# Kernel optimization log

Hardware: AMD Instinct MI355X
Metric: run time of the kernel (lower is better)

Reference implementation:

```python
import jax, jax.numpy as jnp
import numpy as np

B, C, H, W_SP = 4, 64, 64, 64
CI = C // 2  # inter_channels = 32
DEPTH = 64
EPS = 1e-5


def conv2d(x, w, b, pad=0, dil=1):
    out = jax.lax.conv_general_dilated(
        x, w, window_strides=(1, 1),
        padding=[(pad, pad), (pad, pad)],
        rhs_dilation=(dil, dil),
        dimension_numbers=('NCHW', 'OIHW', 'NCHW'))
    return out + b[None, :, None, None]


def setup_inputs() -> dict:
    key = jax.random.key(0)
    ks = iter(jax.random.split(key, 32))
    nrm = lambda shp, s=0.01: jax.random.normal(next(ks), shp, jnp.float32) * s
    inp = {
        'x': jax.random.normal(next(ks), (B, C, H, W_SP), jnp.float32),
        # NonlocalBlock params (init: normal(0, 0.01), bias 0)
        'g_w': nrm((CI, C, 1, 1)), 'g_b': jnp.zeros((CI,), jnp.float32),
        'theta_w': nrm((CI, C, 1, 1)), 'theta_b': jnp.zeros((CI,), jnp.float32),
        'phi_w': nrm((CI, C, 1, 1)), 'phi_b': jnp.zeros((CI,), jnp.float32),
        'Wz_w': nrm((C, CI, 1, 1)), 'Wz_b': jnp.zeros((C,), jnp.float32),
        'bn_g': jax.random.normal(next(ks), (C,), jnp.float32),  # normal_(W[1].weight, 0) -> std 1
        'bn_b': jnp.zeros((C,), jnp.float32),
        # ASPP params (torch default kaiming init approximated by small normals)
        'a_mean_w': nrm((DEPTH, C, 1, 1), 0.05), 'a_mean_b': jnp.zeros((DEPTH,), jnp.float32),
        'a1_w': nrm((DEPTH, C, 1, 1), 0.05), 'a1_b': jnp.zeros((DEPTH,), jnp.float32),
        'a3_w': nrm((DEPTH, C, 3, 3), 0.02), 'a3_b': jnp.zeros((DEPTH,), jnp.float32),
        'a5_w': nrm((DEPTH, C, 3, 3), 0.02), 'a5_b': jnp.zeros((DEPTH,), jnp.float32),
        'a7_w': nrm((DEPTH, C, 3, 3), 0.02), 'a7_b': jnp.zeros((DEPTH,), jnp.float32),
        'out_w': nrm((DEPTH, DEPTH * 5, 1, 1), 0.02), 'out_b': jnp.zeros((DEPTH,), jnp.float32),
    }
    return inp


def _forward(x, g_w, g_b, theta_w, theta_b, phi_w, phi_b, Wz_w, Wz_b, bn_g, bn_b,
             a_mean_w, a_mean_b, a1_w, a1_b, a3_w, a3_b, a5_w, a5_b, a7_w, a7_b,
             out_w, out_b):
    b, c, h, w = x.shape
    n = h * w
    # ---- NonlocalBlock: global self-attention ----
    g_x = conv2d(x, g_w, g_b).reshape(b, CI, n).transpose(0, 2, 1)       # [B,N,Ci]
    theta_x = conv2d(x, theta_w, theta_b).reshape(b, CI, n).transpose(0, 2, 1)  # [B,N,Ci]
    phi_x = conv2d(x, phi_w, phi_b).reshape(b, CI, n)                    # [B,Ci,N]
    f = jnp.einsum('bqc,bck->bqk', theta_x, phi_x)                       # [B,N,N]
    f_div_C = jax.nn.softmax(f, axis=2)
    y = jnp.einsum('bqk,bkc->bqc', f_div_C, g_x)                         # [B,N,Ci]
    y = y.transpose(0, 2, 1).reshape(b, CI, h, w)
    wy = conv2d(y, Wz_w, Wz_b)
    # BatchNorm (eval: running_mean=0, running_var=1)
    wy = wy * (bn_g / jnp.sqrt(1.0 + EPS))[None, :, None, None] + bn_b[None, :, None, None]
    z = wy + x
    # ---- ASPP ----
    img = jnp.mean(z, axis=(2, 3), keepdims=True)                        # [B,C,1,1]
    img = conv2d(img, a_mean_w, a_mean_b)                                # [B,D,1,1]
    img = jnp.broadcast_to(img, (b, DEPTH, h, w))  # bilinear upsample of 1x1 is constant
    b1 = conv2d(z, a1_w, a1_b)
    b3 = conv2d(z, a3_w, a3_b, pad=3, dil=3)
    b5 = conv2d(z, a5_w, a5_b, pad=5, dil=5)
    b7 = conv2d(z, a7_w, a7_b, pad=7, dil=7)
    cat = jnp.concatenate([img, b1, b3, b5, b7], axis=1)                 # [B,5D,H,W]
    return conv2d(cat, out_w, out_b)                                     # [B,D,H,W]


def reference(x, g_w, g_b, theta_w, theta_b, phi_w, phi_b, Wz_w, Wz_b, bn_g, bn_b,
              a_mean_w, a_mean_b, a1_w, a1_b, a3_w, a3_b, a5_w, a5_b, a7_w, a7_b,
              out_w, out_b):
    return _forward(x, g_w, g_b, theta_w, theta_b, phi_w, phi_b, Wz_w, Wz_b, bn_g, bn_b,
                    a_mean_w, a_mean_b, a1_w, a1_b, a3_w, a3_b, a5_w, a5_b, a7_w, a7_b,
                    out_w, out_b)
```

## Files before the change

kernel.cpp:

```cpp
#include <hip/hip_runtime.h>


typedef __attribute__((ext_vector_type(8))) short bf16x8;
typedef __attribute__((ext_vector_type(4))) short s16x4;
typedef __attribute__((ext_vector_type(4))) float f32x4;

#define MFMA(a, b, c) __builtin_amdgcn_mfma_f32_16x16x32_bf16((a), (b), (c), 0, 0, 0)

#if __has_builtin(__builtin_amdgcn_exp2f)
#define EXP2(x) __builtin_amdgcn_exp2f(x)
#else
#define EXP2(x) exp2f(x)
#endif

__device__ static inline short f2bf(float f) {
  union { float f; unsigned u; } v; v.f = f;
  unsigned r = v.u + 0x7fffu + ((v.u >> 16) & 1u);
  return (short)(r >> 16);
}
__device__ static inline float bf2f(unsigned short h) {
  union { unsigned u; float f; } v; v.u = ((unsigned)h) << 16;
  return v.f;
}
__device__ static inline s16x4 pk4(f32x4 v) {
  s16x4 r; r.x = f2bf(v.x); r.y = f2bf(v.y); r.z = f2bf(v.z); r.w = f2bf(v.w);
  return r;
}
__device__ static inline unsigned pk2(float f0, float f1) {
  union { float f; unsigned u; } a, b; a.f = f0; b.f = f1;
  return __builtin_amdgcn_perm(b.u, a.u, 0x07060302u);
}
__device__ static inline f32x4 exp24(f32x4 v) {
  f32x4 r; r.x = EXP2(v.x); r.y = EXP2(v.y); r.z = EXP2(v.z); r.w = EXP2(v.w);
  return r;
}

#define QF_PER_B 131072
#define ZPB      389376
#define LOG2E    1.4426950408889634f

__global__ __launch_bounds__(256) void k_setup(
    const float* __restrict__ x,
    const float* __restrict__ tw, const float* __restrict__ tb,
    const float* __restrict__ pw, const float* __restrict__ pb,
    const float* __restrict__ gw, const float* __restrict__ gb,
    const float* __restrict__ out_w, const float* __restrict__ out_b,
    const float* __restrict__ a1_w, const float* __restrict__ a3_w,
    const float* __restrict__ a5_w, const float* __restrict__ a7_w,
    const float* __restrict__ a1_b, const float* __restrict__ a3_b,
    const float* __restrict__ a5_b, const float* __restrict__ a7_b,
    const float* __restrict__ Wz_w, const float* __restrict__ Wz_b,
    const float* __restrict__ bn_g, const float* __restrict__ bn_b,
    const float* __restrict__ am_w,
    unsigned* __restrict__ zp, float* __restrict__ zmean,
    unsigned short* __restrict__ Wfrag, unsigned short* __restrict__ WzF,
    float* __restrict__ bias2,
    unsigned short* __restrict__ thetaB, unsigned short* __restrict__ phiB,
    unsigned short* __restrict__ gB,
    float* __restrict__ am_wT, float* __restrict__ owT0,
    float* __restrict__ cbias) {
  __shared__ union {
    struct { float wsm[4096]; float osm[64 * 65]; } prep;
    struct { float wl[2048]; float bl[32]; } qkv;
  } sm;
  int blk = blockIdx.x, t = threadIdx.x;
  if (blk < 997) {
    if (blk == 996) { if (t < 256) zmean[t] = 0.f; return; }
    int b = blk / 249, loc = blk - b * 249;
    int i = loc * 256 + t;
    if (i >= 63616) return;
    int px = i >> 5, dw = i & 31;
    int row, col;
    if (px < 1092) {
      int r = px / 78; col = px - r * 78;
      row = (r < 7) ? r : r + 64;
    } else {
      int j = px - 1092;
      int r = j / 14; int c = j - r * 14;
      row = r + 7; col = (c < 7) ? c : c + 57;
    }
    zp[b * (ZPB / 2) + (row * 78 + col) * 32 + dw] = 0u;
  } else if (blk < 1027) {
    int pblk = blk - 997;
    if (pblk < 28) {
      int tap = pblk;
      const float* w; int goff, kyx = 0, ksq = 9;
      if (tap == 0)      { w = a1_w; goff = 64;  ksq = 1; }
      else if (tap < 10) { w = a3_w; goff = 128; kyx = tap - 1; }
      else if (tap < 19) { w = a5_w; goff = 192; kyx = tap - 10; }
      else               { w = a7_w; goff = 256; kyx = tap - 19; }
      for (int i = t; i < 4096; i += 256) {
        sm.prep.wsm[i] = w[i * ksq + kyx];
        int d = i >> 6, m = i & 63;
        sm.prep.osm[d * 65 + m] = out_w[d * 320 + goff + m];
      }
      __syncthreads();
      int dt = t >> 6, lane = t & 63, quad = lane >> 4, l15 = lane & 15;
      int d = dt * 16 + l15;
      float acc[16];
      #pragma unroll
      for (int k = 0; k < 16; ++k) acc[k] = 0.f;
      const float* orow = sm.prep.osm + d * 65;
      int c0 = quad * 8;
      for (int m = 0; m < 64; ++m) {
        float o = orow[m];
        const float* wr = sm.prep.wsm + m * 64 + c0;
        #pragma unroll
        for (int cc = 0; cc < 2; ++cc)
          #pragma unroll
          for (int j = 0; j < 8; ++j)
            acc[cc * 8 + j] += o * wr[cc * 32 + j];
      }
      #pragma unroll
      for (int cc = 0; cc < 2; ++cc) {
        bf16x8 v;
        #pragma unroll
        for (int j = 0; j < 8; ++j) v[j] = f2bf(acc[cc * 8 + j]);
        *(bf16x8*)(Wfrag + (((tap * 4 + dt) * 2 + cc) * 64 + lane) * 8) = v;
      }
    } else if (pblk == 28) {
      int ct = t >> 6, lane = t & 63, quad = lane >> 4, l15 = lane & 15;
      int c = ct * 16 + l15;
      float s = bn_g[c] * rsqrtf(1.f + 1e-5f);
      bf16x8 v;
      #pragma unroll
      for (int j = 0; j < 8; ++j) v[j] = f2bf(s * Wz_w[c * 32 + quad * 8 + j]);
      *(bf16x8*)(WzF + (ct * 64 + lane) * 8) = v;
    } else if (t < 64) {
      float s = bn_g[t] * rsqrtf(1.f + 1e-5f);
      bias2[t] = s * Wz_b[t] + bn_b[t];
    }
  } else if (blk < 1219) {
    int qb = blk - 1027;
    int b = qb & 3, pt = (qb >> 2) & 15, proj = qb >> 6;
    const float* w    = proj == 0 ? tw : (proj == 1 ? pw : gw);
    const float* bias = proj == 0 ? tb : (proj == 1 ? pb : gb);
    for (int i = t; i < 2048; i += 256) sm.qkv.wl[i] = w[i];
    if (t < 32) sm.qkv.bl[t] = bias[t];
    __syncthreads();
    int pix = pt*256 + t;
    const float* xp = x + b*64*4096 + pix;
    float acc[32];
    #pragma unroll
    for (int ci = 0; ci < 32; ++ci) acc[ci] = sm.qkv.bl[ci];
    for (int c = 0; c < 64; ++c) {
      float xv = xp[c*4096];
      #pragma unroll
      for (int ci = 0; ci < 32; ++ci) acc[ci] += sm.qkv.wl[ci*64 + c] * xv;
    }
    if (proj == 0) {
      #pragma unroll
      for (int ci = 0; ci < 32; ++ci) acc[ci] *= LOG2E;
    }
    if (proj < 2) {
      unsigned short* base = (proj == 0 ? thetaB : phiB) + b*QF_PER_B
                             + (pix >> 4)*512 + (pix & 15)*8;
      #pragma unroll
      for (int q = 0; q < 4; ++q) {
        bf16x8 v;
        #pragma unroll
        for (int j = 0; j < 8; ++j) v[j] = f2bf(acc[q*8 + j]);
        *(bf16x8*)(base + q*128) = v;
      }
    } else {
      unsigned short* base = gB + b*QF_PER_B + (pix >> 5)*1024
                             + ((pix & 31) >> 3)*128 + (pix & 7);
      #pragma unroll
      for (int ci = 0; ci < 32; ++ci)
        base[(ci >> 4)*512 + (ci & 15)*8] = (unsigned short)f2bf(acc[ci]);
    }
  } else {
    for (int i = t; i < 4096; i += 256) {
      int d = i >> 6, c = i & 63;
      am_wT[c * 64 + d] = am_w[i];
      owT0[c * 64 + d] = out_w[d * 320 + c];
    }
    if (t < 64) {
      float r = out_b[t];
      const float* ow = out_w + t * 320;
      for (int m = 0; m < 64; ++m)
        r += ow[64 + m] * a1_b[m] + ow[128 + m] * a3_b[m]
           + ow[192 + m] * a5_b[m] + ow[256 + m] * a7_b[m];
      cbias[t] = r;
    }
  }
}

__global__ __launch_bounds__(512) void k_attn(
    const unsigned short* __restrict__ thetaB, const unsigned short* __restrict__ phiB,
    const unsigned short* __restrict__ gB, const unsigned short* __restrict__ WzF,
    const float* __restrict__ bias2, const float* __restrict__ x,
    unsigned short* __restrict__ z_pad, float* __restrict__ zmean) {
  __shared__ float ypart[8][64][20];
  __shared__ __align__(16) unsigned short plds[8][1152];
  __shared__ __align__(16) unsigned short ytr[4][1280];
  int blk = blockIdx.x;
  int b = blk >> 7, qblk = blk & 127;
  int tid = threadIdx.x;
  int kh = tid >> 6, lane = tid & 63, quad = lane >> 4, l15 = lane & 15;
  const bf16x8* thB = (const bf16x8*)(thetaB + b*QF_PER_B);
  const bf16x8* phF = (const bf16x8*)(phiB + b*QF_PER_B);
  const bf16x8* gF  = (const bf16x8*)(gB + b*QF_PER_B);
  bf16x8 th0 = thB[(qblk*2 + 0)*64 + lane];
  bf16x8 th1 = thB[(qblk*2 + 1)*64 + lane];
  bf16x8 ones;
  #pragma unroll
  for (int j = 0; j < 8; ++j) ones[j] = (short)0x3F80;
  const f32x4 z4 = {0.f, 0.f, 0.f, 0.f};
  f32x4 acc00 = z4, acc01 = z4, acc10 = z4, acc11 = z4;
  f32x4 accL0 = z4, accL1 = z4;
  unsigned short* pl = &plds[kh][0];
  unsigned short* r0p = pl + l15*36 + quad*4;
  unsigned short* r1p = pl + 576 + l15*36 + quad*4;
  const unsigned short* q0p = pl + l15*36 + quad*8;
  const unsigned short* q1p = pl + 576 + l15*36 + quad*8;
  int kt0 = kh*16;
  for (int kt = kt0; kt < kt0 + 16; ++kt) {
    int tbase = kt*128 + lane;
    bf16x8 pf0 = phF[tbase];
    bf16x8 pf1 = phF[tbase + 64];
    bf16x8 gf0 = gF[tbase];
    bf16x8 gf1 = gF[tbase + 64];
    f32x4 s00 = MFMA(pf0, th0, z4);
    f32x4 s10 = MFMA(pf1, th0, z4);
    f32x4 s01 = MFMA(pf0, th1, z4);
    f32x4 s11 = MFMA(pf1, th1, z4);
    f32x4 p00 = exp24(s00), p10 = exp24(s10), p01 = exp24(s01), p11 = exp24(s11);
    uint2 w0; w0.x = pk2(p00.x, p00.y); w0.y = pk2(p00.z, p00.w);
    uint2 w1; w1.x = pk2(p10.x, p10.y); w1.y = pk2(p10.z, p10.w);
    uint2 w2; w2.x = pk2(p01.x, p01.y); w2.y = pk2(p01.z, p01.w);
    uint2 w3; w3.x = pk2(p11.x, p11.y); w3.y = pk2(p11.z, p11.w);
    *(uint2*)(r0p)      = w0;
    *(uint2*)(r0p + 16) = w1;
    *(uint2*)(r1p)      = w2;
    *(uint2*)(r1p + 16) = w3;
    uint2 a0 = *(const uint2*)(q0p);
    uint2 a1 = *(const uint2*)(q0p + 4);
    uint2 b0 = *(const uint2*)(q1p);
    uint2 b1 = *(const uint2*)(q1p + 4);
    union { unsigned u[4]; bf16x8 v; } pb0c, pb1c;
    pb0c.u[0] = a0.x; pb0c.u[1] = a0.y; pb0c.u[2] = a1.x; pb0c.u[3] = a1.y;
    pb1c.u[0] = b0.x; pb1c.u[1] = b0.y; pb1c.u[2] = b1.x; pb1c.u[3] = b1.y;
    acc00 = MFMA(gf0, pb0c.v, acc00);
    acc01 = MFMA(gf1, pb0c.v, acc01);
    acc10 = MFMA(gf0, pb1c.v, acc10);
    acc11 = MFMA(gf1, pb1c.v, acc11);
    accL0 = MFMA(ones, pb0c.v, accL0);
    accL1 = MFMA(ones, pb1c.v, accL1);
  }
  float* yp = &ypart[kh][lane][0];
  *(f32x4*)(yp + 0)  = acc00;
  *(f32x4*)(yp + 4)  = acc01;
  *(f32x4*)(yp + 8)  = acc10;
  *(f32x4*)(yp + 12) = acc11;
  yp[16] = accL0.x; yp[17] = accL1.x;
  __syncthreads();
  if (kh >= 4) return;
  int ct = kh;
  f32x4 a00 = z4, a01 = z4, a10 = z4, a11 = z4;
  float l0 = 0.f, l1 = 0.f;
  #pragma unroll
  for (int k = 0; k < 8; ++k) {
    const float* q = &ypart[k][lane][0];
    a00 += *(const f32x4*)(q + 0);
    a01 += *(const f32x4*)(q + 4);
    a10 += *(const f32x4*)(q + 8);
    a11 += *(const f32x4*)(q + 12);
    l0 += q[16]; l1 += q[17];
  }
  float r0 = 1.f / l0, r1 = 1.f / l1;
  a00 *= r0; a01 *= r0; a10 *= r1; a11 *= r1;
  unsigned short* yl = &ytr[ct][0];
  *(s16x4*)(yl + l15*40 + quad*4)             = pk4(a00);
  *(s16x4*)(yl + l15*40 + 16 + quad*4)        = pk4(a01);
  *(s16x4*)(yl + (16 + l15)*40 + quad*4)      = pk4(a10);
  *(s16x4*)(yl + (16 + l15)*40 + 16 + quad*4) = pk4(a11);
  bf16x8 y0 = *(const bf16x8*)(yl + l15*40 + quad*8);
  bf16x8 y1 = *(const bf16x8*)(yl + (16 + l15)*40 + quad*8);
  bf16x8 wf = ((const bf16x8*)WzF)[ct*64 + lane];
  f32x4 zq0 = MFMA(wf, y0, z4);
  f32x4 zq1 = MFMA(wf, y1, z4);
  int c0 = ct*16 + quad*4;
  f32x4 b2 = *(const f32x4*)(bias2 + c0);
  int q0i = qblk * 32;
  const float* xp0 = x + (b*64 + c0)*4096 + q0i + l15;
  f32x4 s0, s1;
  s0.x = zq0.x + b2.x + xp0[0];
  s0.y = zq0.y + b2.y + xp0[4096];
  s0.z = zq0.z + b2.z + xp0[8192];
  s0.w = zq0.w + b2.w + xp0[12288];
  s1.x = zq1.x + b2.x + xp0[16];
  s1.y = zq1.y + b2.y + xp0[4096 + 16];
  s1.z = zq1.z + b2.z + xp0[8192 + 16];
  s1.w = zq1.w + b2.w + xp0[12288 + 16];
  {
    int q = q0i + l15, h = q >> 6, w = q & 63;
    *(s16x4*)(z_pad + b*ZPB + ((h + 7)*78 + (w + 7))*64 + c0) = pk4(s0);
    q = q0i + 16 + l15; h = q >> 6; w = q & 63;
    *(s16x4*)(z_pad + b*ZPB + ((h + 7)*78 + (w + 7))*64 + c0) = pk4(s1);
  }
  f32x4 zs = s0 + s1;
  #pragma unroll
  for (int m = 1; m < 16; m <<= 1) {
    zs.x += __shfl_xor(zs.x, m);
    zs.y += __shfl_xor(zs.y, m);
    zs.z += __shfl_xor(zs.z, m);
    zs.w += __shfl_xor(zs.w, m);
  }
  if (l15 == 0) {
    atomicAdd(zmean + b*64 + c0 + 0, zs.x);
    atomicAdd(zmean + b*64 + c0 + 1, zs.y);
    atomicAdd(zmean + b*64 + c0 + 2, zs.z);
    atomicAdd(zmean + b*64 + c0 + 3, zs.w);
  }
}

__global__ __launch_bounds__(64) void k_conv(
    const unsigned short* __restrict__ z_pad, const unsigned short* __restrict__ Wfrag,
    const float* __restrict__ zmean, const float* __restrict__ am_wT,
    const float* __restrict__ am_b, const float* __restrict__ owT0,
    const float* __restrict__ cbias, float* __restrict__ out) {
  static constexpr int DYt[28] = {0, -3,-3,-3,0,0,0,3,3,3,
                                     -5,-5,-5,0,0,0,5,5,5,
                                     -7,-7,-7,0,0,0,7,7,7};
  static constexpr int DXt[28] = {0, -3,0,3,-3,0,3,-3,0,3,
                                     -5,0,5,-5,0,5,-5,0,5,
                                     -7,0,7,-7,0,7,-7,0,7};
  int blk = blockIdx.x;
  int b = blk >> 8, h = (blk >> 2) & 63, dt2 = (blk >> 1) & 1, wt2 = blk & 1;
  int lane = threadIdx.x, quad = lane >> 4, l15 = lane & 15;
  float zml = zmean[b*64 + lane] * (1.f / 4096.f);
  float img = am_b[lane];
  for (int c = 0; c < 64; ++c) img += am_wT[c*64 + lane] * __shfl(zml, c);
  float cbd = cbias[lane];
  for (int dd = 0; dd < 64; ++dd) cbd += owT0[dd*64 + lane] * __shfl(img, dd);
  const unsigned short* zb = z_pad + b*ZPB + ((h + 7)*78 + 7)*64 + quad*8;
  const bf16x8* wfp = (const bf16x8*)Wfrag + lane;
  int d0 = dt2*2 + 0, d1 = dt2*2 + 1;
  const f32x4 z4 = {0.f, 0.f, 0.f, 0.f};
  f32x4 acc00 = z4, acc01 = z4, acc10 = z4, acc11 = z4;
  int col0 = ((wt2*2 + 0)*16 + l15)*64;
  int col1 = ((wt2*2 + 1)*16 + l15)*64;
  #pragma unroll
  for (int tap = 0; tap < 28; ++tap) {
    int toff = (DYt[tap]*78 + DXt[tap])*64;
    const unsigned short* zrow = zb + toff;
    #pragma unroll
    for (int cc = 0; cc < 2; ++cc) {
      bf16x8 zf0 = *(const bf16x8*)(zrow + col0 + cc*32);
      bf16x8 zf1 = *(const bf16x8*)(zrow + col1 + cc*32);
      bf16x8 wf0 = wfp[((tap*4 + d0)*2 + cc)*64];
      bf16x8 wf1 = wfp[((tap*4 + d1)*2 + cc)*64];
      acc00 = MFMA(wf0, zf0, acc00);
      acc01 = MFMA(wf0, zf1, acc01);
      acc10 = MFMA(wf1, zf0, acc10);
      acc11 = MFMA(wf1, zf1, acc11);
    }
  }
  int dd0 = d0*16 + quad*4, dd1 = d1*16 + quad*4;
  f32x4 cb0v, cb1v;
  cb0v.x = __shfl(cbd, dd0 + 0); cb0v.y = __shfl(cbd, dd0 + 1);
  cb0v.z = __shfl(cbd, dd0 + 2); cb0v.w = __shfl(cbd, dd0 + 3);
  cb1v.x = __shfl(cbd, dd1 + 0); cb1v.y = __shfl(cbd, dd1 + 1);
  cb1v.z = __shfl(cbd, dd1 + 2); cb1v.w = __shfl(cbd, dd1 + 3);
  acc00 += cb0v; acc01 += cb0v; acc10 += cb1v; acc11 += cb1v;
  float* ob = out + b*262144 + h*64;
  int w0 = (wt2*2 + 0)*16 + l15, w1 = (wt2*2 + 1)*16 + l15;
  ob[(dd0 + 0)*4096 + w0] = acc00.x;
  ob[(dd0 + 1)*4096 + w0] = acc00.y;
  ob[(dd0 + 2)*4096 + w0] = acc00.z;
  ob[(dd0 + 3)*4096 + w0] = acc00.w;
  ob[(dd0 + 0)*4096 + w1] = acc01.x;
  ob[(dd0 + 1)*4096 + w1] = acc01.y;
  ob[(dd0 + 2)*4096 + w1] = acc01.z;
  ob[(dd0 + 3)*4096 + w1] = acc01.w;
  ob[(dd1 + 0)*4096 + w0] = acc10.x;
  ob[(dd1 + 1)*4096 + w0] = acc10.y;
  ob[(dd1 + 2)*4096 + w0] = acc10.z;
  ob[(dd1 + 3)*4096 + w0] = acc10.w;
  ob[(dd1 + 0)*4096 + w1] = acc11.x;
  ob[(dd1 + 1)*4096 + w1] = acc11.y;
  ob[(dd1 + 2)*4096 + w1] = acc11.z;
  ob[(dd1 + 3)*4096 + w1] = acc11.w;
}

extern "C" void kernel_launch(void* const* d_in, const int* in_sizes, int n_in,
                              void* d_out, int out_size, void* d_ws, size_t ws_size,
                              hipStream_t stream) {
  const float* x    = (const float*)d_in[0];
  const float* g_w  = (const float*)d_in[1];
  const float* g_b  = (const float*)d_in[2];
  const float* th_w = (const float*)d_in[3];
  const float* th_b = (const float*)d_in[4];
  const float* ph_w = (const float*)d_in[5];
  const float* ph_b = (const float*)d_in[6];
  const float* Wz_w = (const float*)d_in[7];
  const float* Wz_b = (const float*)d_in[8];
  const float* bn_g = (const float*)d_in[9];
  const float* bn_b = (const float*)d_in[10];
  const float* am_w = (const float*)d_in[11];
  const float* am_b = (const float*)d_in[12];
  const float* a1_w = (const float*)d_in[13];
  const float* a1_b = (const float*)d_in[14];
  const float* a3_w = (const float*)d_in[15];
  const float* a3_b = (const float*)d_in[16];
  const float* a5_w = (const float*)d_in[17];
  const float* a5_b = (const float*)d_in[18];
  const float* a7_w = (const float*)d_in[19];
  const float* a7_b = (const float*)d_in[20];
  const float* out_w = (const float*)d_in[21];
  const float* out_b = (const float*)d_in[22];
  float* out = (float*)d_out;
  char* ws = (char*)d_ws;
  unsigned short* thetaB = (unsigned short*)(ws + 0);
  unsigned short* phiB   = (unsigned short*)(ws + 1048576);
  unsigned short* gB     = (unsigned short*)(ws + 2097152);
  unsigned short* z_pad  = (unsigned short*)(ws + 3145728);
  unsigned short* Wfrag  = (unsigned short*)(ws + 6260736);
  unsigned short* WzF    = (unsigned short*)(ws + 6490112);
  float* zmean           = (float*)(ws + 6494208);
  float* bias2           = (float*)(ws + 6495232);
  float* am_wT           = (float*)(ws + 6495488);
  float* owT0            = (float*)(ws + 6511872);
  float* cbias           = (float*)(ws + 6528256);

  k_setup<<<dim3(1220), dim3(256), 0, stream>>>(
      x, th_w, th_b, ph_w, ph_b, g_w, g_b, out_w, out_b,
      a1_w, a3_w, a5_w, a7_w, a1_b, a3_b, a5_b, a7_b,
      Wz_w, Wz_b, bn_g, bn_b, am_w,
      (unsigned*)z_pad, zmean, Wfrag, WzF, bias2,
      thetaB, phiB, gB, am_wT, owT0, cbias);
  k_attn<<<dim3(512), dim3(512), 0, stream>>>(thetaB, phiB, gB, WzF, bias2, x,
                                              z_pad, zmean);
  k_conv<<<dim3(1024), dim3(64), 0, stream>>>(z_pad, Wfrag, zmean, am_wT, am_b,
                                              owT0, cbias, out);
}
```

Measured before the change: 182.2 us.

## Rebalance kernels: fold padding and weight prep into attention, prefetch operands

Replaces the big setup kernel with a small projection kernel. The halo zeroing and ASPP weight folding become extra blocks of the attention kernel, so they run alongside attention work. Adds register double-buffering of phi/g loads in the attention loop and of z_pad loads in the conv loop. The conv kernel is regrouped into 256-thread blocks, one per output row, and the projection kernel batches its x loads. It also fixes the right-halo column index so the zeroing no longer lands on interior columns, which matters now that zeroing runs concurrently with the z writes.

```diff
diff --git a/kernel.cpp b/kernel.cpp
--- a/kernel.cpp
+++ b/kernel.cpp
@@ -18,10 +18,6 @@
   unsigned r = v.u + 0x7fffu + ((v.u >> 16) & 1u);
   return (short)(r >> 16);
 }
-__device__ static inline float bf2f(unsigned short h) {
-  union { unsigned u; float f; } v; v.u = ((unsigned)h) << 16;
-  return v.f;
-}
 __device__ static inline s16x4 pk4(f32x4 v) {
   s16x4 r; r.x = f2bf(v.x); r.y = f2bf(v.y); r.z = f2bf(v.z); r.w = f2bf(v.w);
   return r;
@@ -39,35 +35,226 @@
 #define ZPB      389376
 #define LOG2E    1.4426950408889634f
 
-__global__ __launch_bounds__(256) void k_setup(
+__global__ __launch_bounds__(256) void k_proj(
     const float* __restrict__ x,
     const float* __restrict__ tw, const float* __restrict__ tb,
     const float* __restrict__ pw, const float* __restrict__ pb,
     const float* __restrict__ gw, const float* __restrict__ gb,
+    const float* __restrict__ Wz_w, const float* __restrict__ Wz_b,
+    const float* __restrict__ bn_g, const float* __restrict__ bn_b,
+    unsigned short* __restrict__ thetaB, unsigned short* __restrict__ phiB,
+    unsigned short* __restrict__ gB, unsigned short* __restrict__ WzF,
+    float* __restrict__ bias2, float* __restrict__ zmean) {
+  __shared__ float wl[2048];
+  __shared__ float bl[32];
+  int blk = blockIdx.x, t = threadIdx.x;
+  if (blk < 192) {
+    int b = blk & 3, pt = (blk >> 2) & 15, proj = blk >> 6;
+    const float* w    = proj == 0 ? tw : (proj == 1 ? pw : gw);
+    const float* bias = proj == 0 ? tb : (proj == 1 ? pb : gb);
+    for (int i = t; i < 2048; i += 256) wl[i] = w[i];
+    if (t < 32) bl[t] = bias[t];
+    __syncthreads();
+    int pix = pt*256 + t;
+    const float* xp = x + b*64*4096 + pix;
+    float acc[32];
+    #pragma unroll
+    for (int ci = 0; ci < 32; ++ci) acc[ci] = bl[ci];
+    for (int c0 = 0; c0 < 64; c0 += 16) {
+      float xv[16];
+      #pragma unroll
+      for (int k = 0; k < 16; ++k) xv[k] = xp[(c0 + k)*4096];
+      #pragma unroll
+      for (int k = 0; k < 16; ++k)
+        #pragma unroll
+        for (int ci = 0; ci < 32; ++ci) acc[ci] += wl[ci*64 + c0 + k] * xv[k];
+    }
+    if (proj == 0) {
+      #pragma unroll
+      for (int ci = 0; ci < 32; ++ci) acc[ci] *= LOG2E;
+    }
+    if (proj < 2) {
+      unsigned short* base = (proj == 0 ? thetaB : phiB) + b*QF_PER_B
+                             + (pix >> 4)*512 + (pix & 15)*8;
+      #pragma unroll
+      for (int q = 0; q < 4; ++q) {
+        bf16x8 v;
+        #pragma unroll
+        for (int j = 0; j < 8; ++j) v[j] = f2bf(acc[q*8 + j]);
+        *(bf16x8*)(base + q*128) = v;
+      }
+    } else {
+      unsigned short* base = gB + b*QF_PER_B + (pix >> 5)*1024
+                             + ((pix & 31) >> 3)*128 + (pix & 7);
+      #pragma unroll
+      for (int ci = 0; ci < 32; ++ci)
+        base[(ci >> 4)*512 + (ci & 15)*8] = (unsigned short)f2bf(acc[ci]);
+    }
+  } else if (blk == 192) {
+    int ct = t >> 6, lane = t & 63, quad = lane >> 4, l15 = lane & 15;
+    int c = ct * 16 + l15;
+    float s = bn_g[c] * rsqrtf(1.f + 1e-5f);
+    bf16x8 v;
+    #pragma unroll
+    for (int j = 0; j < 8; ++j) v[j] = f2bf(s * Wz_w[c * 32 + quad * 8 + j]);
+    *(bf16x8*)(WzF + (ct * 64 + lane) * 8) = v;
+    if (t < 64) {
+      float s2 = bn_g[t] * rsqrtf(1.f + 1e-5f);
+      bias2[t] = s2 * Wz_b[t] + bn_b[t];
+    }
+  } else {
+    zmean[t] = 0.f;
+  }
+}
+
+__global__ __launch_bounds__(512, 4) void k_attn(
+    const unsigned short* __restrict__ thetaB, const unsigned short* __restrict__ phiB,
+    const unsigned short* __restrict__ gB, const unsigned short* __restrict__ WzF,
+    const float* __restrict__ bias2, const float* __restrict__ x,
+    unsigned short* __restrict__ z_pad, float* __restrict__ zmean,
     const float* __restrict__ out_w, const float* __restrict__ out_b,
     const float* __restrict__ a1_w, const float* __restrict__ a3_w,
     const float* __restrict__ a5_w, const float* __restrict__ a7_w,
     const float* __restrict__ a1_b, const float* __restrict__ a3_b,
     const float* __restrict__ a5_b, const float* __restrict__ a7_b,
-    const float* __restrict__ Wz_w, const float* __restrict__ Wz_b,
-    const float* __restrict__ bn_g, const float* __restrict__ bn_b,
     const float* __restrict__ am_w,
-    unsigned* __restrict__ zp, float* __restrict__ zmean,
-    unsigned short* __restrict__ Wfrag, unsigned short* __restrict__ WzF,
-    float* __restrict__ bias2,
-    unsigned short* __restrict__ thetaB, unsigned short* __restrict__ phiB,
-    unsigned short* __restrict__ gB,
-    float* __restrict__ am_wT, float* __restrict__ owT0,
-    float* __restrict__ cbias) {
+    unsigned short* __restrict__ Wfrag, float* __restrict__ am_wT,
+    float* __restrict__ owT0, float* __restrict__ cbias) {
   __shared__ union {
+    struct {
+      float ypart[8][64][20];
+      unsigned short plds[8][1152];
+      unsigned short ytr[4][1280];
+    } attn;
     struct { float wsm[4096]; float osm[64 * 65]; } prep;
-    struct { float wl[2048]; float bl[32]; } qkv;
   } sm;
-  int blk = blockIdx.x, t = threadIdx.x;
-  if (blk < 997) {
-    if (blk == 996) { if (t < 256) zmean[t] = 0.f; return; }
-    int b = blk / 249, loc = blk - b * 249;
-    int i = loc * 256 + t;
+  int blk = blockIdx.x, tid = threadIdx.x;
+  if (blk < 512) {
+    int b = blk >> 7, qblk = blk & 127;
+    int kh = tid >> 6, lane = tid & 63, quad = lane >> 4, l15 = lane & 15;
+    const bf16x8* thB = (const bf16x8*)(thetaB + b*QF_PER_B);
+    const bf16x8* phF = (const bf16x8*)(phiB + b*QF_PER_B);
+    const bf16x8* gF  = (const bf16x8*)(gB + b*QF_PER_B);
+    bf16x8 th0 = thB[(qblk*2 + 0)*64 + lane];
+    bf16x8 th1 = thB[(qblk*2 + 1)*64 + lane];
+    bf16x8 ones;
+    #pragma unroll
+    for (int j = 0; j < 8; ++j) ones[j] = (short)0x3F80;
+    const f32x4 z4 = {0.f, 0.f, 0.f, 0.f};
+    f32x4 acc00 = z4, acc01 = z4, acc10 = z4, acc11 = z4;
+    f32x4 accL0 = z4, accL1 = z4;
+    unsigned short* pl = &sm.attn.plds[kh][0];
+    unsigned short* r0p = pl + l15*36 + quad*4;
+    unsigned short* r1p = pl + 576 + l15*36 + quad*4;
+    const unsigned short* q0p = pl + l15*36 + quad*8;
+    const unsigned short* q1p = pl + 576 + l15*36 + quad*8;
+    int kt0 = kh*16;
+    int tb0 = kt0*128 + lane;
+    bf16x8 pf0 = phF[tb0], pf1 = phF[tb0 + 64];
+    bf16x8 gf0 = gF[tb0],  gf1 = gF[tb0 + 64];
+    for (int kt = kt0; kt < kt0 + 16; ++kt) {
+      bf16x8 cp0 = pf0, cp1 = pf1, cg0 = gf0, cg1 = gf1;
+      if (kt + 1 < kt0 + 16) {
+        int tb = (kt + 1)*128 + lane;
+        pf0 = phF[tb]; pf1 = phF[tb + 64];
+        gf0 = gF[tb];  gf1 = gF[tb + 64];
+      }
+      f32x4 s00 = MFMA(cp0, th0, z4);
+      f32x4 s10 = MFMA(cp1, th0, z4);
+      f32x4 s01 = MFMA(cp0, th1, z4);
+      f32x4 s11 = MFMA(cp1, th1, z4);
+      f32x4 p00 = exp24(s00), p10 = exp24(s10), p01 = exp24(s01), p11 = exp24(s11);
+      uint2 w0; w0.x = pk2(p00.x, p00.y); w0.y = pk2(p00.z, p00.w);
+      uint2 w1; w1.x = pk2(p10.x, p10.y); w1.y = pk2(p10.z, p10.w);
+      uint2 w2; w2.x = pk2(p01.x, p01.y); w2.y = pk2(p01.z, p01.w);
+      uint2 w3; w3.x = pk2(p11.x, p11.y); w3.y = pk2(p11.z, p11.w);
+      *(uint2*)(r0p)      = w0;
+      *(uint2*)(r0p + 16) = w1;
+      *(uint2*)(r1p)      = w2;
+      *(uint2*)(r1p + 16) = w3;
+      uint2 a0 = *(const uint2*)(q0p);
+      uint2 a1 = *(const uint2*)(q0p + 4);
+      uint2 b0 = *(const uint2*)(q1p);
+      uint2 b1 = *(const uint2*)(q1p + 4);
+      union { unsigned u[4]; bf16x8 v; } pb0c, pb1c;
+      pb0c.u[0] = a0.x; pb0c.u[1] = a0.y; pb0c.u[2] = a1.x; pb0c.u[3] = a1.y;
+      pb1c.u[0] = b0.x; pb1c.u[1] = b0.y; pb1c.u[2] = b1.x; pb1c.u[3] = b1.y;
+      acc00 = MFMA(cg0, pb0c.v, acc00);
+      acc01 = MFMA(cg1, pb0c.v, acc01);
+      acc10 = MFMA(cg0, pb1c.v, acc10);
+      acc11 = MFMA(cg1, pb1c.v, acc11);
+      accL0 = MFMA(ones, pb0c.v, accL0);
+      accL1 = MFMA(ones, pb1c.v, accL1);
+    }
+    float* yp = &sm.attn.ypart[kh][lane][0];
+    *(f32x4*)(yp + 0)  = acc00;
+    *(f32x4*)(yp + 4)  = acc01;
+    *(f32x4*)(yp + 8)  = acc10;
+    *(f32x4*)(yp + 12) = acc11;
+    yp[16] = accL0.x; yp[17] = accL1.x;
+    __syncthreads();
+    if (kh >= 4) return;
+    int ct = kh;
+    f32x4 a00 = z4, a01 = z4, a10 = z4, a11 = z4;
+    float l0 = 0.f, l1 = 0.f;
+    #pragma unroll
+    for (int k = 0; k < 8; ++k) {
+      const float* q = &sm.attn.ypart[k][lane][0];
+      a00 += *(const f32x4*)(q + 0);
+      a01 += *(const f32x4*)(q + 4);
+      a10 += *(const f32x4*)(q + 8);
+      a11 += *(const f32x4*)(q + 12);
+      l0 += q[16]; l1 += q[17];
+    }
+    float r0 = 1.f / l0, r1 = 1.f / l1;
+    a00 *= r0; a01 *= r0; a10 *= r1; a11 *= r1;
+    unsigned short* yl = &sm.attn.ytr[ct][0];
+    *(s16x4*)(yl + l15*40 + quad*4)             = pk4(a00);
+    *(s16x4*)(yl + l15*40 + 16 + quad*4)        = pk4(a01);
+    *(s16x4*)(yl + (16 + l15)*40 + quad*4)      = pk4(a10);
+    *(s16x4*)(yl + (16 + l15)*40 + 16 + quad*4) = pk4(a11);
+    bf16x8 y0 = *(const bf16x8*)(yl + l15*40 + quad*8);
+    bf16x8 y1 = *(const bf16x8*)(yl + (16 + l15)*40 + quad*8);
+    bf16x8 wf = ((const bf16x8*)WzF)[ct*64 + lane];
+    f32x4 zq0 = MFMA(wf, y0, z4);
+    f32x4 zq1 = MFMA(wf, y1, z4);
+    int c0 = ct*16 + quad*4;
+    f32x4 b2 = *(const f32x4*)(bias2 + c0);
+    int q0i = qblk * 32;
+    const float* xp0 = x + (b*64 + c0)*4096 + q0i + l15;
+    f32x4 s0, s1;
+    s0.x = zq0.x + b2.x + xp0[0];
+    s0.y = zq0.y + b2.y + xp0[4096];
+    s0.z = zq0.z + b2.z + xp0[8192];
+    s0.w = zq0.w + b2.w + xp0[12288];
+    s1.x = zq1.x + b2.x + xp0[16];
+    s1.y = zq1.y + b2.y + xp0[4096 + 16];
+    s1.z = zq1.z + b2.z + xp0[8192 + 16];
+    s1.w = zq1.w + b2.w + xp0[12288 + 16];
+    {
+      int q = q0i + l15, h = q >> 6, w = q & 63;
+      *(s16x4*)(z_pad + b*ZPB + ((h + 7)*78 + (w + 7))*64 + c0) = pk4(s0);
+      q = q0i + 16 + l15; h = q >> 6; w = q & 63;
+      *(s16x4*)(z_pad + b*ZPB + ((h + 7)*78 + (w + 7))*64 + c0) = pk4(s1);
+    }
+    f32x4 zs = s0 + s1;
+    #pragma unroll
+    for (int m = 1; m < 16; m <<= 1) {
+      zs.x += __shfl_xor(zs.x, m);
+      zs.y += __shfl_xor(zs.y, m);
+      zs.z += __shfl_xor(zs.z, m);
+      zs.w += __shfl_xor(zs.w, m);
+    }
+    if (l15 == 0) {
+      atomicAdd(zmean + b*64 + c0 + 0, zs.x);
+      atomicAdd(zmean + b*64 + c0 + 1, zs.y);
+      atomicAdd(zmean + b*64 + c0 + 2, zs.z);
+      atomicAdd(zmean + b*64 + c0 + 3, zs.w);
+    }
+  } else if (blk < 1012) {
+    int hb = blk - 512;
+    int b = hb / 125, loc = hb - b * 125;
+    int i = loc * 512 + tid;
     if (i >= 63616) return;
     int px = i >> 5, dw = i & 31;
     int row, col;
@@ -77,245 +264,63 @@
     } else {
       int j = px - 1092;
       int r = j / 14; int c = j - r * 14;
-      row = r + 7; col = (c < 7) ? c : c + 57;
-    }
-    zp[b * (ZPB / 2) + (row * 78 + col) * 32 + dw] = 0u;
-  } else if (blk < 1027) {
-    int pblk = blk - 997;
-    if (pblk < 28) {
-      int tap = pblk;
-      const float* w; int goff, kyx = 0, ksq = 9;
-      if (tap == 0)      { w = a1_w; goff = 64;  ksq = 1; }
-      else if (tap < 10) { w = a3_w; goff = 128; kyx = tap - 1; }
-      else if (tap < 19) { w = a5_w; goff = 192; kyx = tap - 10; }
-      else               { w = a7_w; goff = 256; kyx = tap - 19; }
-      for (int i = t; i < 4096; i += 256) {
-        sm.prep.wsm[i] = w[i * ksq + kyx];
-        int d = i >> 6, m = i & 63;
-        sm.prep.osm[d * 65 + m] = out_w[d * 320 + goff + m];
-      }
-      __syncthreads();
-      int dt = t >> 6, lane = t & 63, quad = lane >> 4, l15 = lane & 15;
-      int d = dt * 16 + l15;
-      float acc[16];
-      #pragma unroll
-      for (int k = 0; k < 16; ++k) acc[k] = 0.f;
-      const float* orow = sm.prep.osm + d * 65;
-      int c0 = quad * 8;
-      for (int m = 0; m < 64; ++m) {
-        float o = orow[m];
-        const float* wr = sm.prep.wsm + m * 64 + c0;
+      row = r + 7; col = (c < 7) ? c : c + 64;
+    }
+    ((unsigned*)z_pad)[b * (ZPB / 2) + (row * 78 + col) * 32 + dw] = 0u;
+  } else if (blk < 1040) {
+    int tap = blk - 1012;
+    const float* w; int goff, kyx = 0, ksq = 9;
+    if (tap == 0)      { w = a1_w; goff = 64;  ksq = 1; }
+    else if (tap < 10) { w = a3_w; goff = 128; kyx = tap - 1; }
+    else if (tap < 19) { w = a5_w; goff = 192; kyx = tap - 10; }
+    else               { w = a7_w; goff = 256; kyx = tap - 19; }
+    for (int i = tid; i < 4096; i += 512) {
+      sm.prep.wsm[i] = w[i * ksq + kyx];
+      int d = i >> 6, m = i & 63;
+      sm.prep.osm[d * 65 + m] = out_w[d * 320 + goff + m];
+    }
+    __syncthreads();
+    int dt = (tid >> 6) & 3, lane = tid & 63, quad = lane >> 4, l15 = lane & 15;
+    int d = dt * 16 + l15;
+    float acc[16];
+    #pragma unroll
+    for (int k = 0; k < 16; ++k) acc[k] = 0.f;
+    const float* orow = sm.prep.osm + d * 65;
+    int c0 = quad * 8;
+    for (int m = 0; m < 64; ++m) {
+      float o = orow[m];
+      const float* wr = sm.prep.wsm + m * 64 + c0;
+      #pragma unroll
+      for (int cc = 0; cc < 2; ++cc)
         #pragma unroll
-        for (int cc = 0; cc < 2; ++cc)
-          #pragma unroll
-          for (int j = 0; j < 8; ++j)
-            acc[cc * 8 + j] += o * wr[cc * 32 + j];
-      }
-      #pragma unroll
-      for (int cc = 0; cc < 2; ++cc) {
-        bf16x8 v;
-        #pragma unroll
-        for (int j = 0; j < 8; ++j) v[j] = f2bf(acc[cc * 8 + j]);
-        *(bf16x8*)(Wfrag + (((tap * 4 + dt) * 2 + cc) * 64 + lane) * 8) = v;
-      }
-    } else if (pblk == 28) {
-      int ct = t >> 6, lane = t & 63, quad = lane >> 4, l15 = lane & 15;
-      int c = ct * 16 + l15;
-      float s = bn_g[c] * rsqrtf(1.f + 1e-5f);
+        for (int j = 0; j < 8; ++j)
+          acc[cc * 8 + j] += o * wr[cc * 32 + j];
+    }
+    #pragma unroll
+    for (int cc = 0; cc < 2; ++cc) {
       bf16x8 v;
       #pragma unroll
-      for (int j = 0; j < 8; ++j) v[j] = f2bf(s * Wz_w[c * 32 + quad * 8 + j]);
-      *(bf16x8*)(WzF + (ct * 64 + lane) * 8) = v;
-    } else if (t < 64) {
-      float s = bn_g[t] * rsqrtf(1.f + 1e-5f);
-      bias2[t] = s * Wz_b[t] + bn_b[t];
-    }
-  } else if (blk < 1219) {
-    int qb = blk - 1027;
-    int b = qb & 3, pt = (qb >> 2) & 15, proj = qb >> 6;
-    const float* w    = proj == 0 ? tw : (proj == 1 ? pw : gw);
-    const float* bias = proj == 0 ? tb : (proj == 1 ? pb : gb);
-    for (int i = t; i < 2048; i += 256) sm.qkv.wl[i] = w[i];
-    if (t < 32) sm.qkv.bl[t] = bias[t];
-    __syncthreads();
-    int pix = pt*256 + t;
-    const float* xp = x + b*64*4096 + pix;
-    float acc[32];
-    #pragma unroll
-    for (int ci = 0; ci < 32; ++ci) acc[ci] = sm.qkv.bl[ci];
-    for (int c = 0; c < 64; ++c) {
-      float xv = xp[c*4096];
-      #pragma unroll
-      for (int ci = 0; ci < 32; ++ci) acc[ci] += sm.qkv.wl[ci*64 + c] * xv;
-    }
-    if (proj == 0) {
-      #pragma unroll
-      for (int ci = 0; ci < 32; ++ci) acc[ci] *= LOG2E;
-    }
-    if (proj < 2) {
-      unsigned short* base = (proj == 0 ? thetaB : phiB) + b*QF_PER_B
-                             + (pix >> 4)*512 + (pix & 15)*8;
-      #pragma unroll
-      for (int q = 0; q < 4; ++q) {
-        bf16x8 v;
-        #pragma unroll
-        for (int j = 0; j < 8; ++j) v[j] = f2bf(acc[q*8 + j]);
-        *(bf16x8*)(base + q*128) = v;
-      }
-    } else {
-      unsigned short* base = gB + b*QF_PER_B + (pix >> 5)*1024
-                             + ((pix & 31) >> 3)*128 + (pix & 7);
-      #pragma unroll
-      for (int ci = 0; ci < 32; ++ci)
-        base[(ci >> 4)*512 + (ci & 15)*8] = (unsigned short)f2bf(acc[ci]);
+      for (int j = 0; j < 8; ++j) v[j] = f2bf(acc[cc * 8 + j]);
+      *(bf16x8*)(Wfrag + (((tap * 4 + dt) * 2 + cc) * 64 + lane) * 8) = v;
     }
   } else {
-    for (int i = t; i < 4096; i += 256) {
+    for (int i = tid; i < 4096; i += 512) {
       int d = i >> 6, c = i & 63;
       am_wT[c * 64 + d] = am_w[i];
       owT0[c * 64 + d] = out_w[d * 320 + c];
     }
-    if (t < 64) {
-      float r = out_b[t];
-      const float* ow = out_w + t * 320;
+    if (tid < 64) {
+      float r = out_b[tid];
+      const float* ow = out_w + tid * 320;
       for (int m = 0; m < 64; ++m)
         r += ow[64 + m] * a1_b[m] + ow[128 + m] * a3_b[m]
            + ow[192 + m] * a5_b[m] + ow[256 + m] * a7_b[m];
-      cbias[t] = r;
+      cbias[tid] = r;
     }
   }
 }
 
-__global__ __launch_bounds__(512) void k_attn(
-    const unsigned short* __restrict__ thetaB, const unsigned short* __restrict__ phiB,
-    const unsigned short* __restrict__ gB, const unsigned short* __restrict__ WzF,
-    const float* __restrict__ bias2, const float* __restrict__ x,
-    unsigned short* __restrict__ z_pad, float* __restrict__ zmean) {
-  __shared__ float ypart[8][64][20];
-  __shared__ __align__(16) unsigned short plds[8][1152];
-  __shared__ __align__(16) unsigned short ytr[4][1280];
-  int blk = blockIdx.x;
-  int b = blk >> 7, qblk = blk & 127;
-  int tid = threadIdx.x;
-  int kh = tid >> 6, lane = tid & 63, quad = lane >> 4, l15 = lane & 15;
-  const bf16x8* thB = (const bf16x8*)(thetaB + b*QF_PER_B);
-  const bf16x8* phF = (const bf16x8*)(phiB + b*QF_PER_B);
-  const bf16x8* gF  = (const bf16x8*)(gB + b*QF_PER_B);
-  bf16x8 th0 = thB[(qblk*2 + 0)*64 + lane];
-  bf16x8 th1 = thB[(qblk*2 + 1)*64 + lane];
-  bf16x8 ones;
-  #pragma unroll
-  for (int j = 0; j < 8; ++j) ones[j] = (short)0x3F80;
-  const f32x4 z4 = {0.f, 0.f, 0.f, 0.f};
-  f32x4 acc00 = z4, acc01 = z4, acc10 = z4, acc11 = z4;
-  f32x4 accL0 = z4, accL1 = z4;
-  unsigned short* pl = &plds[kh][0];
-  unsigned short* r0p = pl + l15*36 + quad*4;
-  unsigned short* r1p = pl + 576 + l15*36 + quad*4;
-  const unsigned short* q0p = pl + l15*36 + quad*8;
-  const unsigned short* q1p = pl + 576 + l15*36 + quad*8;
-  int kt0 = kh*16;
-  for (int kt = kt0; kt < kt0 + 16; ++kt) {
-    int tbase = kt*128 + lane;
-    bf16x8 pf0 = phF[tbase];
-    bf16x8 pf1 = phF[tbase + 64];
-    bf16x8 gf0 = gF[tbase];
-    bf16x8 gf1 = gF[tbase + 64];
-    f32x4 s00 = MFMA(pf0, th0, z4);
-    f32x4 s10 = MFMA(pf1, th0, z4);
-    f32x4 s01 = MFMA(pf0, th1, z4);
-    f32x4 s11 = MFMA(pf1, th1, z4);
-    f32x4 p00 = exp24(s00), p10 = exp24(s10), p01 = exp24(s01), p11 = exp24(s11);
-    uint2 w0; w0.x = pk2(p00.x, p00.y); w0.y = pk2(p00.z, p00.w);
-    uint2 w1; w1.x = pk2(p10.x, p10.y); w1.y = pk2(p10.z, p10.w);
-    uint2 w2; w2.x = pk2(p01.x, p01.y); w2.y = pk2(p01.z, p01.w);
-    uint2 w3; w3.x = pk2(p11.x, p11.y); w3.y = pk2(p11.z, p11.w);
-    *(uint2*)(r0p)      = w0;
-    *(uint2*)(r0p + 16) = w1;
-    *(uint2*)(r1p)      = w2;
-    *(uint2*)(r1p + 16) = w3;
-    uint2 a0 = *(const uint2*)(q0p);
-    uint2 a1 = *(const uint2*)(q0p + 4);
-    uint2 b0 = *(const uint2*)(q1p);
-    uint2 b1 = *(const uint2*)(q1p + 4);
-    union { unsigned u[4]; bf16x8 v; } pb0c, pb1c;
-    pb0c.u[0] = a0.x; pb0c.u[1] = a0.y; pb0c.u[2] = a1.x; pb0c.u[3] = a1.y;
-    pb1c.u[0] = b0.x; pb1c.u[1] = b0.y; pb1c.u[2] = b1.x; pb1c.u[3] = b1.y;
-    acc00 = MFMA(gf0, pb0c.v, acc00);
-    acc01 = MFMA(gf1, pb0c.v, acc01);
-    acc10 = MFMA(gf0, pb1c.v, acc10);
-    acc11 = MFMA(gf1, pb1c.v, acc11);
-    accL0 = MFMA(ones, pb0c.v, accL0);
-    accL1 = MFMA(ones, pb1c.v, accL1);
-  }
-  float* yp = &ypart[kh][lane][0];
-  *(f32x4*)(yp + 0)  = acc00;
-  *(f32x4*)(yp + 4)  = acc01;
-  *(f32x4*)(yp + 8)  = acc10;
-  *(f32x4*)(yp + 12) = acc11;
-  yp[16] = accL0.x; yp[17] = accL1.x;
-  __syncthreads();
-  if (kh >= 4) return;
-  int ct = kh;
-  f32x4 a00 = z4, a01 = z4, a10 = z4, a11 = z4;
-  float l0 = 0.f, l1 = 0.f;
-  #pragma unroll
-  for (int k = 0; k < 8; ++k) {
-    const float* q = &ypart[k][lane][0];
-    a00 += *(const f32x4*)(q + 0);
-    a01 += *(const f32x4*)(q + 4);
-    a10 += *(const f32x4*)(q + 8);
-    a11 += *(const f32x4*)(q + 12);
-    l0 += q[16]; l1 += q[17];
-  }
-  float r0 = 1.f / l0, r1 = 1.f / l1;
-  a00 *= r0; a01 *= r0; a10 *= r1; a11 *= r1;
-  unsigned short* yl = &ytr[ct][0];
-  *(s16x4*)(yl + l15*40 + quad*4)             = pk4(a00);
-  *(s16x4*)(yl + l15*40 + 16 + quad*4)        = pk4(a01);
-  *(s16x4*)(yl + (16 + l15)*40 + quad*4)      = pk4(a10);
-  *(s16x4*)(yl + (16 + l15)*40 + 16 + quad*4) = pk4(a11);
-  bf16x8 y0 = *(const bf16x8*)(yl + l15*40 + quad*8);
-  bf16x8 y1 = *(const bf16x8*)(yl + (16 + l15)*40 + quad*8);
-  bf16x8 wf = ((const bf16x8*)WzF)[ct*64 + lane];
-  f32x4 zq0 = MFMA(wf, y0, z4);
-  f32x4 zq1 = MFMA(wf, y1, z4);
-  int c0 = ct*16 + quad*4;
-  f32x4 b2 = *(const f32x4*)(bias2 + c0);
-  int q0i = qblk * 32;
-  const float* xp0 = x + (b*64 + c0)*4096 + q0i + l15;
-  f32x4 s0, s1;
-  s0.x = zq0.x + b2.x + xp0[0];
-  s0.y = zq0.y + b2.y + xp0[4096];
-  s0.z = zq0.z + b2.z + xp0[8192];
-  s0.w = zq0.w + b2.w + xp0[12288];
-  s1.x = zq1.x + b2.x + xp0[16];
-  s1.y = zq1.y + b2.y + xp0[4096 + 16];
-  s1.z = zq1.z + b2.z + xp0[8192 + 16];
-  s1.w = zq1.w + b2.w + xp0[12288 + 16];
-  {
-    int q = q0i + l15, h = q >> 6, w = q & 63;
-    *(s16x4*)(z_pad + b*ZPB + ((h + 7)*78 + (w + 7))*64 + c0) = pk4(s0);
-    q = q0i + 16 + l15; h = q >> 6; w = q & 63;
-    *(s16x4*)(z_pad + b*ZPB + ((h + 7)*78 + (w + 7))*64 + c0) = pk4(s1);
-  }
-  f32x4 zs = s0 + s1;
-  #pragma unroll
-  for (int m = 1; m < 16; m <<= 1) {
-    zs.x += __shfl_xor(zs.x, m);
-    zs.y += __shfl_xor(zs.y, m);
-    zs.z += __shfl_xor(zs.z, m);
-    zs.w += __shfl_xor(zs.w, m);
-  }
-  if (l15 == 0) {
-    atomicAdd(zmean + b*64 + c0 + 0, zs.x);
-    atomicAdd(zmean + b*64 + c0 + 1, zs.y);
-    atomicAdd(zmean + b*64 + c0 + 2, zs.z);
-    atomicAdd(zmean + b*64 + c0 + 3, zs.w);
-  }
-}
-
-__global__ __launch_bounds__(64) void k_conv(
+__global__ __launch_bounds__(256, 4) void k_conv(
     const unsigned short* __restrict__ z_pad, const unsigned short* __restrict__ Wfrag,
     const float* __restrict__ zmean, const float* __restrict__ am_wT,
     const float* __restrict__ am_b, const float* __restrict__ owT0,
@@ -327,8 +332,10 @@
                                      -5,0,5,-5,0,5,-5,0,5,
                                      -7,0,7,-7,0,7,-7,0,7};
   int blk = blockIdx.x;
-  int b = blk >> 8, h = (blk >> 2) & 63, dt2 = (blk >> 1) & 1, wt2 = blk & 1;
-  int lane = threadIdx.x, quad = lane >> 4, l15 = lane & 15;
+  int b = blk >> 6, h = blk & 63;
+  int tid = threadIdx.x;
+  int wave = tid >> 6, lane = tid & 63, quad = lane >> 4, l15 = lane & 15;
+  int dt2 = wave >> 1, wt2 = wave & 1;
   float zml = zmean[b*64 + lane] * (1.f / 4096.f);
   float img = am_b[lane];
   for (int c = 0; c < 64; ++c) img += am_wT[c*64 + lane] * __shfl(zml, c);
@@ -341,21 +348,24 @@
   f32x4 acc00 = z4, acc01 = z4, acc10 = z4, acc11 = z4;
   int col0 = ((wt2*2 + 0)*16 + l15)*64;
   int col1 = ((wt2*2 + 1)*16 + l15)*64;
+  bf16x8 zf0 = *(const bf16x8*)(zb + (DYt[0]*78 + DXt[0])*64 + col0);
+  bf16x8 zf1 = *(const bf16x8*)(zb + (DYt[0]*78 + DXt[0])*64 + col1);
   #pragma unroll
-  for (int tap = 0; tap < 28; ++tap) {
-    int toff = (DYt[tap]*78 + DXt[tap])*64;
-    const unsigned short* zrow = zb + toff;
-    #pragma unroll
-    for (int cc = 0; cc < 2; ++cc) {
-      bf16x8 zf0 = *(const bf16x8*)(zrow + col0 + cc*32);
-      bf16x8 zf1 = *(const bf16x8*)(zrow + col1 + cc*32);
-      bf16x8 wf0 = wfp[((tap*4 + d0)*2 + cc)*64];
-      bf16x8 wf1 = wfp[((tap*4 + d1)*2 + cc)*64];
-      acc00 = MFMA(wf0, zf0, acc00);
-      acc01 = MFMA(wf0, zf1, acc01);
-      acc10 = MFMA(wf1, zf0, acc10);
-      acc11 = MFMA(wf1, zf1, acc11);
-    }
+  for (int idx = 0; idx < 56; ++idx) {
+    int tap = idx >> 1, cc = idx & 1;
+    bf16x8 c0v = zf0, c1v = zf1;
+    if (idx < 55) {
+      int ntap = (idx + 1) >> 1, ncc = (idx + 1) & 1;
+      const unsigned short* nz = zb + (DYt[ntap]*78 + DXt[ntap])*64 + ncc*32;
+      zf0 = *(const bf16x8*)(nz + col0);
+      zf1 = *(const bf16x8*)(nz + col1);
+    }
+    bf16x8 wf0 = wfp[((tap*4 + d0)*2 + cc)*64];
+    bf16x8 wf1 = wfp[((tap*4 + d1)*2 + cc)*64];
+    acc00 = MFMA(wf0, c0v, acc00);
+    acc01 = MFMA(wf0, c1v, acc01);
+    acc10 = MFMA(wf1, c0v, acc10);
+    acc11 = MFMA(wf1, c1v, acc11);
   }
   int dd0 = d0*16 + quad*4, dd1 = d1*16 + quad*4;
   f32x4 cb0v, cb1v;
@@ -424,14 +434,13 @@
   float* owT0            = (float*)(ws + 6511872);
   float* cbias           = (float*)(ws + 6528256);
 
-  k_setup<<<dim3(1220), dim3(256), 0, stream>>>(
-      x, th_w, th_b, ph_w, ph_b, g_w, g_b, out_w, out_b,
-      a1_w, a3_w, a5_w, a7_w, a1_b, a3_b, a5_b, a7_b,
-      Wz_w, Wz_b, bn_g, bn_b, am_w,
-      (unsigned*)z_pad, zmean, Wfrag, WzF, bias2,
-      thetaB, phiB, gB, am_wT, owT0, cbias);
-  k_attn<<<dim3(512), dim3(512), 0, stream>>>(thetaB, phiB, gB, WzF, bias2, x,
-                                              z_pad, zmean);
-  k_conv<<<dim3(1024), dim3(64), 0, stream>>>(z_pad, Wfrag, zmean, am_wT, am_b,
+  k_proj<<<dim3(194), dim3(256), 0, stream>>>(
+      x, th_w, th_b, ph_w, ph_b, g_w, g_b, Wz_w, Wz_b, bn_g, bn_b,
+      thetaB, phiB, gB, WzF, bias2, zmean);
+  k_attn<<<dim3(1041), dim3(512), 0, stream>>>(
+      thetaB, phiB, gB, WzF, bias2, x, z_pad, zmean,
+      out_w, out_b, a1_w, a3_w, a5_w, a7_w, a1_b, a3_b, a5_b, a7_b, am_w,
+      Wfrag, am_wT, owT0, cbias);
+  k_conv<<<dim3(256), dim3(256), 0, stream>>>(z_pad, Wfrag, zmean, am_wT, am_b,
                                               owT0, cbias, out);
 }
```

Result: slower. 189.5 us (+4.0%).
